# Performance work log

Hardware: AMD Instinct MI355X
Metric: run time of the kernel (lower is better)

The kernel has to match this reference:

```python
import jax, jax.numpy as jnp
import numpy as np

MU = 1e-4          # mu from __init__ (divide-by-zero guard)
COUNT_EPS = 1e-4   # epsilon added to per-partition counts
TWO_PI = 2.0 * np.pi


def setup_inputs() -> dict:
    key = jax.random.key(0)
    k1, k2 = jax.random.split(key)
    trajs = jax.random.normal(k1, (8192, 8, 2), dtype=jnp.float32)
    nei_trajs = jax.random.normal(k2, (8192, 128, 8, 2), dtype=jnp.float32)
    return {"trajs": trajs, "nei_trajs": nei_trajs, "partitions": 8}


def reference(trajs, nei_trajs, partitions):
    # trajs: [B, T, 2]; nei_trajs: [B, N, T, 2]
    obs_vec = trajs[..., -1, :] - trajs[..., 0, :]            # [B, 2]
    nei_vec = nei_trajs[..., -1, :] - nei_trajs[..., 0, :]    # [B, N, 2]
    nei_len = jnp.linalg.norm(nei_vec, axis=-1)               # [B, N]
    obs_len = jnp.linalg.norm(obs_vec, axis=-1)               # [B]
    # relative_velocity=True branch
    f_speed = (nei_len + MU) / (obs_len[..., None] + MU)      # [B, N]

    nei_pos = nei_trajs[..., -1, :] - trajs[..., None, -1, :]  # [B, N, 2]
    f_distance = jnp.linalg.norm(nei_pos, axis=-1)             # [B, N]
    # tf.atan2(x=v0, y=v1) == atan2(y=v1, x=v0)
    f_direction = jnp.mod(jnp.arctan2(nei_pos[..., 1], nei_pos[..., 0]), TWO_PI)

    angle_idx = (f_direction / (TWO_PI / partitions)).astype(jnp.int32)  # [B, N]
    # neighbor validity mask: sum over time+coord axes nonzero
    nei_mask = (jnp.sum(nei_trajs, axis=(-1, -2)) != 0).astype(jnp.int32)
    angle_idx = angle_idx * nei_mask - (1 - nei_mask)  # invalid -> -1

    # one-hot bucketization fuses the per-partition masked means into one pass;
    # one_hot maps index -1 to an all-zero row, matching the mask-out semantics.
    oh = jax.nn.one_hot(angle_idx, partitions, dtype=f_speed.dtype)  # [B, N, P]
    counts = jnp.sum(oh, axis=1) + COUNT_EPS                          # [B, P]

    feats = jnp.stack([f_speed, f_distance, f_direction], axis=-1)    # [B, N, 3]
    social_circle = jnp.einsum('bnf,bnp->bpf', feats, oh) / counts[..., None]  # [B, P, 3]
    # max_partitions == partitions -> no padding
    return social_circle, f_direction
```

## Files before the change

### kernel.cpp

```cpp
#include <hip/hip_runtime.h>
#include <math.h>

#define MU 1e-4f
#define COUNT_EPS 1e-4f
#define TWO_PI_F 6.28318530717958647692f
#define PI_F 3.14159265358979323846f
#define HALF_PI_F 1.57079632679489661923f

constexpr int P   = 8;
constexpr int N   = 128;
constexpr int WPB = 4;
constexpr int RPW = 2;

template <int CTRL>
__device__ __forceinline__ float dpp_add(float v) {
    int m = __builtin_amdgcn_update_dpp(0, __float_as_int(v), CTRL, 0xF, 0xF, true);
    return v + __int_as_float(m);
}
__device__ __forceinline__ float wave_sum(float v) {
    v = dpp_add<0x111>(v);
    v = dpp_add<0x112>(v);
    v = dpp_add<0x114>(v);
    v = dpp_add<0x118>(v);
    v = dpp_add<0x142>(v);
    v = dpp_add<0x143>(v);
    return v;
}

__device__ __forceinline__ float atan2_2pi(float y, float x) {
    const float ax = fabsf(x), ay = fabsf(y);
    const float mx = fmaxf(ax, ay), mn = fminf(ax, ay);
    const float t  = mn * __builtin_amdgcn_rcpf(fmaxf(mx, 1e-30f));
    const float t2 = t * t;
    float a = fmaf(t2, 0.0208351f, -0.0851330f);
    a = fmaf(t2, a, 0.1801410f);
    a = fmaf(t2, a, -0.3302995f);
    a = fmaf(t2, a, 0.9998660f);
    a *= t;
    a = (ay > ax) ? (HALF_PI_F - a) : a;
    a = (x < 0.0f) ? (PI_F - a) : a;
    return (y < 0.0f) ? (TWO_PI_F - a) : a;
}

struct Feat { float spd, dst, dir; int idx; };

__device__ __forceinline__ Feat features(const float4* c, float robs,
                                          float lx, float ly, float inv_step) {
    Feat f;
    const float4 v0 = c[0], v1 = c[1], v2 = c[2], v3 = c[3];
    const float msum = ((v0.x + v0.y) + (v0.z + v0.w))
                     + ((v1.x + v1.y) + (v1.z + v1.w))
                     + ((v2.x + v2.y) + (v2.z + v2.w))
                     + ((v3.x + v3.y) + (v3.z + v3.w));
    const float ex = v3.z, ey = v3.w;
    const float nvx = ex - v0.x, nvy = ey - v0.y;
    f.spd = (__builtin_amdgcn_sqrtf(fmaf(nvx, nvx, nvy * nvy)) + MU) * robs;
    const float px = ex - lx, py = ey - ly;
    f.dst = __builtin_amdgcn_sqrtf(fmaf(px, px, py * py));
    f.dir = atan2_2pi(py, px);
    const int idx = (int)(f.dir * inv_step);
    f.idx = ((msum != 0.0f) && (idx < P)) ? idx : -1;
    return f;
}

__device__ __forceinline__ void process_row(
    size_t b, const float4* c0, const float4* c1,
    const float* __restrict__ trajs, float* __restrict__ social,
    float* __restrict__ fdir, int lane, float inv_step)
{
    const float* tb = trajs + b * 16;
    const float lx = tb[14], ly = tb[15];
    const float ox = lx - tb[0], oy = ly - tb[1];
    const float robs = __builtin_amdgcn_rcpf(
        __builtin_amdgcn_sqrtf(fmaf(ox, ox, oy * oy)) + MU);

    const Feat f0 = features(c0, robs, lx, ly, inv_step);
    const Feat f1 = features(c1, robs, lx, ly, inv_step);

    fdir[b * N + lane]      = f0.dir;
    fdir[b * N + 64 + lane] = f1.dir;

    float4 o[6];
    #pragma unroll
    for (int p = 0; p < P; ++p) {
        const bool m0 = (f0.idx == p);
        const bool m1 = (f1.idx == p);
        const int cnt = __popcll(__ballot(m0)) + __popcll(__ballot(m1));
        const float rc = __builtin_amdgcn_rcpf((float)cnt + COUNT_EPS);
        const float s_spd = wave_sum((m0 ? f0.spd : 0.0f) + (m1 ? f1.spd : 0.0f));
        const float s_dst = wave_sum((m0 ? f0.dst : 0.0f) + (m1 ? f1.dst : 0.0f));
        const float s_dir = wave_sum((m0 ? f0.dir : 0.0f) + (m1 ? f1.dir : 0.0f));
        const int k = p * 3;
        ((float*)o)[k + 0] = s_spd * rc;
        ((float*)o)[k + 1] = s_dst * rc;
        ((float*)o)[k + 2] = s_dir * rc;
    }

    if (lane == 63) {
        float4* sp = (float4*)(social + b * (P * 3));
        #pragma unroll
        for (int j = 0; j < 6; ++j) sp[j] = o[j];
    }
}

__global__ __launch_bounds__(256) void social_circle_kernel(
    const float* __restrict__ trajs,
    const float* __restrict__ nei,
    float* __restrict__ social,
    float* __restrict__ fdir,
    int B)
{
    const int lane = threadIdx.x & 63;
    const int wib  = threadIdx.x >> 6;
    const int wave = blockIdx.x * WPB + wib;
    const size_t b0 = (size_t)wave * RPW;
    if (b0 >= (size_t)B) return;

    const float inv_step = 1.0f / (TWO_PI_F / (float)P);

    const float4* baseA = (const float4*)(nei + b0 * (N * 16));
    float4 a0[4], a1[4];
    #pragma unroll
    for (int k = 0; k < 4; ++k) a0[k] = baseA[lane * 4 + k];
    #pragma unroll
    for (int k = 0; k < 4; ++k) a1[k] = baseA[(lane + 64) * 4 + k];

    const bool has1 = (b0 + 1 < (size_t)B);
    float4 b0r[4], b1r[4];
    if (has1) {
        const float4* baseB = (const float4*)(nei + (b0 + 1) * (N * 16));
        #pragma unroll
        for (int k = 0; k < 4; ++k) b0r[k] = baseB[lane * 4 + k];
        #pragma unroll
        for (int k = 0; k < 4; ++k) b1r[k] = baseB[(lane + 64) * 4 + k];
    }

    process_row(b0, a0, a1, trajs, social, fdir, lane, inv_step);
    if (has1) process_row(b0 + 1, b0r, b1r, trajs, social, fdir, lane, inv_step);
}

extern "C" void kernel_launch(void* const* d_in, const int* in_sizes, int n_in,
                              void* d_out, int out_size, void* d_ws, size_t ws_size,
                              hipStream_t stream) {
    const float* trajs = (const float*)d_in[0];
    const float* nei   = (const float*)d_in[1];
    const int B = in_sizes[0] / 16;

    float* social = (float*)d_out;
    float* fdir   = (float*)d_out + (size_t)B * P * 3;

    const int waves  = (B + RPW - 1) / RPW;
    const int blocks = (waves + WPB - 1) / WPB;
    social_circle_kernel<<<blocks, WPB * 64, 0, stream>>>(trajs, nei, social, fdir, B);
}
```

Baseline: 20.57 us.

## Double-buffer neighbor rows through LDS via async global-to-LDS loads

```diff
diff --git a/kernel.cpp b/kernel.cpp
--- a/kernel.cpp
+++ b/kernel.cpp
@@ -10,7 +10,7 @@
 constexpr int P   = 8;
 constexpr int N   = 128;
 constexpr int WPB = 4;
-constexpr int RPW = 2;
+constexpr int RPW = 4;
 
 template <int CTRL>
 __device__ __forceinline__ float dpp_add(float v) {
@@ -63,10 +63,30 @@
     return f;
 }
 
+__device__ __forceinline__ int slot(int n, int c) {
+    return (n << 2) | (c ^ ((n >> 1) & 3));
+}
+
+__device__ __forceinline__ void gload_lds16(const float4* g, float4* l) {
+    __builtin_amdgcn_global_load_lds(
+        (const __attribute__((address_space(1))) void*)g,
+        (__attribute__((address_space(3))) void*)l, 16, 0, 0);
+}
+
+__device__ __forceinline__ void stage_row(const float4* rowbase, float4* buf,
+                                          int lane) {
+    #pragma unroll
+    for (int k = 0; k < 8; ++k) {
+        const int s = k * 64 + lane;
+        const int g = s ^ ((s >> 3) & 3);
+        gload_lds16(rowbase + g, buf + k * 64);
+    }
+}
+
 __device__ __forceinline__ void process_row(
-    size_t b, const float4* c0, const float4* c1,
-    const float* __restrict__ trajs, float* __restrict__ social,
-    float* __restrict__ fdir, int lane, float inv_step)
+    size_t b, const float4* buf, const float* __restrict__ trajs,
+    float* __restrict__ social, float* __restrict__ fdir,
+    int lane, float inv_step)
 {
     const float* tb = trajs + b * 16;
     const float lx = tb[14], ly = tb[15];
@@ -74,7 +94,14 @@
     const float robs = __builtin_amdgcn_rcpf(
         __builtin_amdgcn_sqrtf(fmaf(ox, ox, oy * oy)) + MU);
 
+    float4 c0[4];
+    #pragma unroll
+    for (int c = 0; c < 4; ++c) c0[c] = buf[slot(lane, c)];
     const Feat f0 = features(c0, robs, lx, ly, inv_step);
+
+    float4 c1[4];
+    #pragma unroll
+    for (int c = 0; c < 4; ++c) c1[c] = buf[256 + slot(lane, c)];
     const Feat f1 = features(c1, robs, lx, ly, inv_step);
 
     fdir[b * N + lane]      = f0.dir;
@@ -113,30 +140,29 @@
     const int lane = threadIdx.x & 63;
     const int wib  = threadIdx.x >> 6;
     const int wave = blockIdx.x * WPB + wib;
+
+    __shared__ float4 stage_s[WPB][2][512];
+
+    const float inv_step = 1.0f / (TWO_PI_F / (float)P);
     const size_t b0 = (size_t)wave * RPW;
     if (b0 >= (size_t)B) return;
 
-    const float inv_step = 1.0f / (TWO_PI_F / (float)P);
+    stage_row((const float4*)(nei + b0 * (N * 16)), stage_s[wib][0], lane);
 
-    const float4* baseA = (const float4*)(nei + b0 * (N * 16));
-    float4 a0[4], a1[4];
     #pragma unroll
-    for (int k = 0; k < 4; ++k) a0[k] = baseA[lane * 4 + k];
-    #pragma unroll
-    for (int k = 0; k < 4; ++k) a1[k] = baseA[(lane + 64) * 4 + k];
+    for (int r = 0; r < RPW; ++r) {
+        const size_t b = b0 + r;
+        if (b >= (size_t)B) break;
 
-    const bool has1 = (b0 + 1 < (size_t)B);
-    float4 b0r[4], b1r[4];
-    if (has1) {
-        const float4* baseB = (const float4*)(nei + (b0 + 1) * (N * 16));
-        #pragma unroll
-        for (int k = 0; k < 4; ++k) b0r[k] = baseB[lane * 4 + k];
-        #pragma unroll
-        for (int k = 0; k < 4; ++k) b1r[k] = baseB[(lane + 64) * 4 + k];
+        asm volatile("s_waitcnt vmcnt(0)" ::: "memory");
+        __builtin_amdgcn_sched_barrier(0);
+
+        if (r + 1 < RPW && b + 1 < (size_t)B)
+            stage_row((const float4*)(nei + (b + 1) * (N * 16)),
+                      stage_s[wib][(r + 1) & 1], lane);
+
+        process_row(b, stage_s[wib][r & 1], trajs, social, fdir, lane, inv_step);
     }
-
-    process_row(b0, a0, a1, trajs, social, fdir, lane, inv_step);
-    if (has1) process_row(b0 + 1, b0r, b1r, trajs, social, fdir, lane, inv_step);
 }
 
 extern "C" void kernel_launch(void* const* d_in, const int* in_sizes, int n_in,
```

After: 20.24 us. Within noise of the previous version (-1.6%).
